# Performance work log

Hardware: AMD Instinct MI355X
Metric: run time of the kernel (lower is better)

Reference implementation:

```python
import jax, jax.numpy as jnp
import numpy as np

NOISE_LEVEL = 0.05
GAMMA = 0.2  # dt/tau


def setup_inputs() -> dict:
    key = jax.random.key(0)
    ks = jax.random.split(key, 4)
    B, T, I, L, O = 64, 512, 128, 1024, 128
    return {
        "input": jax.random.normal(ks[0], (B, T, I), dtype=jnp.float32),
        "noise": jax.random.normal(ks[1], (B, T, L), dtype=jnp.float32),
        "wi": jax.random.normal(ks[2], (I, L), dtype=jnp.float32),
        "si": jnp.ones((I,), dtype=jnp.float32),
        "wrec": jax.random.normal(ks[3], (L, L), dtype=jnp.float32) * (1.0 / np.sqrt(L)),
        "b": jnp.zeros((L,), dtype=jnp.float32),
        "wo": jax.random.normal(jax.random.fold_in(key, 7), (L, O), dtype=jnp.float32) * (1.0 / L),
        "so": jnp.ones((O,), dtype=jnp.float32),
        "h0": jnp.zeros((L,), dtype=jnp.float32),
    }


def reference(input, noise, wi, si, wrec, b, wo, so, h0):
    B = input.shape[0]
    # proxy parameters: wi_full = (wi.T * si).T == wi * si[:, None]; wo_full = wo * so
    wi_full = wi * si[:, None]          # (I, L)
    wo_full = wo * so                   # (L, O)

    h_init = jnp.broadcast_to(h0, (B, h0.shape[0]))  # (B, L)
    r_init = jnp.tanh(h_init)

    # Precompute input projections for all steps (no sequential dependency).
    u = jnp.einsum('bti,il->btl', input, wi_full)     # (B, T, L)

    def step(carry, xs):
        h, r = carry
        u_t, n_t = xs                                 # (B, L), (B, L)
        h = h + NOISE_LEVEL * n_t + GAMMA * (-h + r @ wrec.T + u_t)
        r = jnp.tanh(h + b)
        out_t = jnp.tanh(h) @ wo_full                 # (B, O)
        return (h, r), out_t

    xs = (jnp.swapaxes(u, 0, 1), jnp.swapaxes(noise, 0, 1))  # time-major
    _, out_t = jax.lax.scan(step, (h_init, r_init), xs)
    return jnp.swapaxes(out_t, 0, 1)                 # (B, T, O)
```

## Files before the change

### kernel.cpp

```cpp
#include <hip/hip_runtime.h>
#include <hip/hip_bf16.h>
#include <cstdint>
#include <cstddef>


static constexpr int B = 64, T = 512, I = 128, L = 1024, O = 128;
static constexpr float C_NOISE = 0.05f, C_GAMMA = 0.2f;

static constexpr int NROW = 4, BT = 16, NJB = 16, JT = 64;

static constexpr size_t WREC_OFF = 0;
static constexpr size_t WIT_OFF  = WREC_OFF + (size_t)L * L * 2;
static constexpr size_t WOT_OFF  = WIT_OFF + (size_t)L * I * 2;
static constexpr size_t RBUF_OFF = WOT_OFF + (size_t)O * L * 2;
static constexpr size_t FLAG_OFF = RBUF_OFF + (size_t)2 * B * L * 2;
static constexpr size_t NFLAGS   = (size_t)NROW * (T + 1) * NJB * 4;
static constexpr size_t FLAG_BYTES = NFLAGS * 4;
static constexpr size_t HBUF_OFF = ((FLAG_OFF + FLAG_BYTES + 511) / 512) * 512;
static constexpr size_t WS_NEED  = HBUF_OFF + (size_t)B * T * L * 2;

typedef __attribute__((ext_vector_type(8))) short s16x8;
typedef __attribute__((ext_vector_type(4))) float f32x4;
typedef __attribute__((ext_vector_type(4))) unsigned int u32x4;
typedef __attribute__((ext_vector_type(2))) unsigned long long u64x2;

__device__ __forceinline__ float fexp2(float x) {
#if __has_builtin(__builtin_amdgcn_exp2f)
  return __builtin_amdgcn_exp2f(x);
#else
  return exp2f(x);
#endif
}
__device__ __forceinline__ float frcp(float x) {
#if __has_builtin(__builtin_amdgcn_rcpf)
  return __builtin_amdgcn_rcpf(x);
#else
  return 1.0f / x;
#endif
}
__device__ __forceinline__ float fast_tanh(float x) {
  float e = fexp2(x * 2.8853900817779268f);
  return 1.0f - 2.0f * frcp(e + 1.0f);
}
__device__ __forceinline__ uint16_t bf16bits(float x) {
  __hip_bfloat16 h = __float2bfloat16(x);
  return *reinterpret_cast<uint16_t*>(&h);
}

__global__ void pack_kernel(const float* __restrict__ wi, const float* __restrict__ si,
                            const float* __restrict__ wrec,
                            const float* __restrict__ wo, const float* __restrict__ so,
                            uint8_t* __restrict__ ws) {
  int idx = blockIdx.x * blockDim.x + threadIdx.x;
  int stride = gridDim.x * blockDim.x;

  __hip_bfloat16* wrecb = (__hip_bfloat16*)(ws + WREC_OFF);
  for (int i = idx; i < L * L; i += stride) wrecb[i] = __float2bfloat16(wrec[i]);

  __hip_bfloat16* wit = (__hip_bfloat16*)(ws + WIT_OFF);
  for (int n = idx; n < L * I; n += stride) {
    int l = n >> 7, ii = n & 127;
    wit[n] = __float2bfloat16(wi[(size_t)ii * L + l] * si[ii]);
  }
  __hip_bfloat16* wot = (__hip_bfloat16*)(ws + WOT_OFF);
  for (int n = idx; n < O * L; n += stride) {
    int o = n >> 10, l = n & 1023;
    wot[n] = __float2bfloat16(wo[(size_t)l * O + o] * so[o]);
  }
  uint32_t* flags = (uint32_t*)(ws + FLAG_OFF);
  for (size_t n = idx; n < NFLAGS; n += stride) flags[n] = 0;
}

__launch_bounds__(256, 1)
__global__ void rnn_kernel(const float* __restrict__ input, const float* __restrict__ noise,
                           const float* __restrict__ bvec, const float* __restrict__ h0,
                           uint8_t* __restrict__ ws) {
  const int tid  = threadIdx.x;
  const int lane = tid & 63;
  const int w    = tid >> 6;
  const int bx   = blockIdx.x;
  const int row  = bx & 3;
  const int jblk = bx >> 2;
  const int b0   = row * BT;
  const int j0   = jblk * JT;
  const int l15  = lane & 15;
  const int lhi  = lane >> 4;

  const int jc0  = j0 + w * 16 + lhi * 4;
  const int mybatch = b0 + l15;

  const short* wrecb = (const short*)(ws + WREC_OFF);
  const short* wit   = (const short*)(ws + WIT_OFF);
  uint64_t* rbuf     = (uint64_t*)(ws + RBUF_OFF);
  uint32_t* flags    = (uint32_t*)(ws + FLAG_OFF);
  __hip_bfloat16* hbuf = (__hip_bfloat16*)(ws + HBUF_OFF);

  __shared__ __align__(16) uint8_t ldsA[2][16 * 2048];

  s16x8 wfrag[32];
  #pragma unroll
  for (int kt = 0; kt < 32; ++kt)
    wfrag[kt] = *(const s16x8*)(wrecb + (size_t)(j0 + w * 16 + l15) * L + kt * 32 + lhi * 8);
  s16x8 wifrag[4];
  #pragma unroll
  for (int kt = 0; kt < 4; ++kt)
    wifrag[kt] = *(const s16x8*)(wit + (size_t)(j0 + w * 16 + l15) * I + kt * 32 + lhi * 8);

  f32x4 bias, h;
  #pragma unroll
  for (int q = 0; q < 4; ++q) { bias[q] = bvec[jc0 + q]; h[q] = h0[jc0 + q]; }

  const int grow = tid >> 4;
  const int gseg = tid & 15;
  const int gsw  = (grow ^ gseg) & 7;

  {
    uint64_t pv = 0;
    #pragma unroll
    for (int q = 0; q < 4; ++q)
      pv |= (uint64_t)bf16bits(fast_tanh(h0[jc0 + q])) << (16 * q);
    size_t slot = (size_t)mybatch * (L / 4) + (size_t)(jc0 >> 2);
    __hip_atomic_store(&rbuf[slot], pv, __ATOMIC_RELAXED, __HIP_MEMORY_SCOPE_AGENT);
    __builtin_amdgcn_s_waitcnt(0);
    if (lane == 0)
      __hip_atomic_store(&flags[((size_t)(row * (T + 1) + 0) * NJB + jblk) * 4 + w], 1u,
                         __ATOMIC_RELAXED, __HIP_MEMORY_SCOPE_AGENT);
  }

  for (int t = 0; t < T; ++t) {
    f32x4 inLo[4], inHi[4];
    #pragma unroll
    for (int kt = 0; kt < 4; ++kt) {
      const float* p = input + ((size_t)(b0 + l15) * T + t) * I + kt * 32 + lhi * 8;
      inLo[kt] = *(const f32x4*)p;
      inHi[kt] = *(const f32x4*)(p + 4);
    }
    f32x4 nz = *(const f32x4*)(noise + ((size_t)mybatch * T + t) * L + jc0);
    s16x8 af[4];
    #pragma unroll
    for (int kt = 0; kt < 4; ++kt)
      #pragma unroll
      for (int q = 0; q < 4; ++q) {
        af[kt][q]     = (short)bf16bits(inLo[kt][q]);
        af[kt][q + 4] = (short)bf16bits(inHi[kt][q]);
      }

    f32x4 acc0 = {0.f,0.f,0.f,0.f}, acc1 = {0.f,0.f,0.f,0.f};
    f32x4 acc2 = {0.f,0.f,0.f,0.f}, acc3 = {0.f,0.f,0.f,0.f};
    acc0 = __builtin_amdgcn_mfma_f32_16x16x32_bf16(wifrag[0], af[0], acc0, 0, 0, 0);
    acc1 = __builtin_amdgcn_mfma_f32_16x16x32_bf16(wifrag[1], af[1], acc1, 0, 0, 0);
    acc2 = __builtin_amdgcn_mfma_f32_16x16x32_bf16(wifrag[2], af[2], acc2, 0, 0, 0);
    acc3 = __builtin_amdgcn_mfma_f32_16x16x32_bf16(wifrag[3], af[3], acc3, 0, 0, 0);

    {
      const uint32_t* fp = flags + ((size_t)(row * (T + 1) + t) * NJB + gseg) * 4;
      u32x4 f4;
      do {
        asm volatile("global_load_dwordx4 %0, %1, off sc0 sc1\n\ts_waitcnt vmcnt(0)"
                     : "=&v"(f4) : "v"(fp) : "memory");
      } while ((f4.x & f4.y & f4.z & f4.w) == 0u);
    }

    {
      const uint8_t* src = (const uint8_t*)rbuf
                         + (size_t)(t & 1) * (B * L * 2)
                         + (size_t)(b0 + grow) * 2048 + (size_t)gseg * 128;
      u64x2 v[8];
      #pragma unroll
      for (int i = 0; i < 8; ++i)
        asm volatile("global_load_dwordx4 %0, %1, off sc0 sc1"
                     : "=&v"(v[i]) : "v"(src + i * 16) : "memory");
      asm volatile("s_waitcnt vmcnt(0)" ::: "memory");
      __builtin_amdgcn_sched_barrier(0);
      uint8_t* dst = ldsA[t & 1] + grow * 2048 + gseg * 128;
      #pragma unroll
      for (int i = 0; i < 8; ++i)
        *(u64x2*)(dst + ((i ^ gsw) * 16)) = v[i];
    }
    __syncthreads();

    const uint8_t* Ab = ldsA[t & 1];
    #pragma unroll
    for (int kt = 0; kt < 32; ++kt) {
      int slot = ((kt * 4 + lhi) ^ ((l15 ^ (kt >> 1)) & 7)) * 16;
      s16x8 a = *(const s16x8*)(Ab + l15 * 2048 + slot);
      switch (kt & 3) {
        case 0: acc0 = __builtin_amdgcn_mfma_f32_16x16x32_bf16(wfrag[kt], a, acc0, 0, 0, 0); break;
        case 1: acc1 = __builtin_amdgcn_mfma_f32_16x16x32_bf16(wfrag[kt], a, acc1, 0, 0, 0); break;
        case 2: acc2 = __builtin_amdgcn_mfma_f32_16x16x32_bf16(wfrag[kt], a, acc2, 0, 0, 0); break;
        default: acc3 = __builtin_amdgcn_mfma_f32_16x16x32_bf16(wfrag[kt], a, acc3, 0, 0, 0); break;
      }
    }

    uint64_t pv = 0;
    #pragma unroll
    for (int q = 0; q < 4; ++q) {
      float hn = 0.8f * h[q] + C_GAMMA * ((acc0[q] + acc1[q]) + (acc2[q] + acc3[q]))
               + C_NOISE * nz[q];
      h[q] = hn;
      pv |= (uint64_t)bf16bits(fast_tanh(hn + bias[q])) << (16 * q);
    }
    {
      size_t slot = (size_t)((t + 1) & 1) * (B * L / 4)
                  + (size_t)mybatch * (L / 4) + (size_t)(jc0 >> 2);
      __hip_atomic_store(&rbuf[slot], pv, __ATOMIC_RELAXED, __HIP_MEMORY_SCOPE_AGENT);
    }
    __builtin_amdgcn_s_waitcnt(0);
    if (lane == 0)
      __hip_atomic_store(&flags[((size_t)(row * (T + 1) + (t + 1)) * NJB + jblk) * 4 + w], 1u,
                         __ATOMIC_RELAXED, __HIP_MEMORY_SCOPE_AGENT);

    {
      uint64_t hv = 0;
      #pragma unroll
      for (int q = 0; q < 4; ++q)
        hv |= (uint64_t)bf16bits(fast_tanh(h[q])) << (16 * q);
      *(uint64_t*)(hbuf + ((size_t)mybatch * T + t) * L + jc0) = hv;
    }
  }
}

__launch_bounds__(256)
__global__ void out_gemm(const uint8_t* __restrict__ ws, float* __restrict__ out) {
  const short* hs  = (const short*)(ws + HBUF_OFF);
  const short* wot = (const short*)(ws + WOT_OFF);
  const int tid = threadIdx.x, lane = tid & 63, w = tid >> 6;
  const int wm = w >> 1, wn = w & 1;
  const int l15 = lane & 15, lhi = lane >> 4;
  const size_t m0 = (size_t)blockIdx.x * 128 + (size_t)wm * 64;

  f32x4 acc[4][4] = {};
  for (int kt = 0; kt < 32; ++kt) {
    s16x8 a[4], b[4];
    #pragma unroll
    for (int fi = 0; fi < 4; ++fi)
      a[fi] = *(const s16x8*)(hs + (m0 + fi * 16 + l15) * L + kt * 32 + lhi * 8);
    #pragma unroll
    for (int fj = 0; fj < 4; ++fj)
      b[fj] = *(const s16x8*)(wot + (size_t)(wn * 64 + fj * 16 + l15) * L + kt * 32 + lhi * 8);
    #pragma unroll
    for (int fi = 0; fi < 4; ++fi)
      #pragma unroll
      for (int fj = 0; fj < 4; ++fj)
        acc[fi][fj] = __builtin_amdgcn_mfma_f32_16x16x32_bf16(a[fi], b[fj], acc[fi][fj], 0, 0, 0);
  }
  #pragma unroll
  for (int fi = 0; fi < 4; ++fi)
    #pragma unroll
    for (int fj = 0; fj < 4; ++fj)
      #pragma unroll
      for (int q = 0; q < 4; ++q) {
        size_t m = m0 + fi * 16 + lhi * 4 + q;
        out[m * O + wn * 64 + fj * 16 + l15] = acc[fi][fj][q];
      }
}

__global__ void ws_too_small(float* out, int n) {
  int i = blockIdx.x * blockDim.x + threadIdx.x;
  if (i < n) out[i] = 12345.0f;
}

extern "C" void kernel_launch(void* const* d_in, const int* in_sizes, int n_in,
                              void* d_out, int out_size, void* d_ws, size_t ws_size,
                              hipStream_t stream) {
  const float* input = (const float*)d_in[0];
  const float* noise = (const float*)d_in[1];
  const float* wi    = (const float*)d_in[2];
  const float* si    = (const float*)d_in[3];
  const float* wrec  = (const float*)d_in[4];
  const float* bvec  = (const float*)d_in[5];
  const float* wo    = (const float*)d_in[6];
  const float* so    = (const float*)d_in[7];
  const float* h0    = (const float*)d_in[8];
  uint8_t* ws = (uint8_t*)d_ws;
  float* out = (float*)d_out;

  if (ws_size < WS_NEED) {
    ws_too_small<<<(out_size + 255) / 256, 256, 0, stream>>>(out, out_size);
    return;
  }

  pack_kernel<<<256, 256, 0, stream>>>(wi, si, wrec, wo, so, ws);
  rnn_kernel<<<NROW * NJB, 256, 0, stream>>>(input, noise, bvec, h0, ws);
  out_gemm<<<(B * T) / 128, 256, 0, stream>>>(ws, out);
}
```

Baseline: 2.060 ms.

## Embed sequence-parity bit in recurrent state words, drop separate flag array

Replaces the per-step flag array and its spin-wait with data-embedded validity. The low bit of each packed bf16 state word now carries a phase bit, and consumers re-poll the state buffer until every word shows the expected phase. This removes the waitcnt-then-flag-store on the producer side and one round trip of flag polling on the consumer side. In exchange it perturbs the least significant mantissa bit of one bf16 value per word, and the spin loop has an iteration cap that could let stale data through.

```diff
diff --git a/kernel.cpp b/kernel.cpp
--- a/kernel.cpp
+++ b/kernel.cpp
@@ -13,15 +13,12 @@
 static constexpr size_t WIT_OFF  = WREC_OFF + (size_t)L * L * 2;
 static constexpr size_t WOT_OFF  = WIT_OFF + (size_t)L * I * 2;
 static constexpr size_t RBUF_OFF = WOT_OFF + (size_t)O * L * 2;
-static constexpr size_t FLAG_OFF = RBUF_OFF + (size_t)2 * B * L * 2;
-static constexpr size_t NFLAGS   = (size_t)NROW * (T + 1) * NJB * 4;
-static constexpr size_t FLAG_BYTES = NFLAGS * 4;
-static constexpr size_t HBUF_OFF = ((FLAG_OFF + FLAG_BYTES + 511) / 512) * 512;
+static constexpr size_t RBUF_BYTES = (size_t)2 * B * L * 2;
+static constexpr size_t HBUF_OFF = ((RBUF_OFF + RBUF_BYTES + 131072 + 511) / 512) * 512;
 static constexpr size_t WS_NEED  = HBUF_OFF + (size_t)B * T * L * 2;
 
 typedef __attribute__((ext_vector_type(8))) short s16x8;
 typedef __attribute__((ext_vector_type(4))) float f32x4;
-typedef __attribute__((ext_vector_type(4))) unsigned int u32x4;
 typedef __attribute__((ext_vector_type(2))) unsigned long long u64x2;
 
 __device__ __forceinline__ float fexp2(float x) {
@@ -67,8 +64,8 @@
     int o = n >> 10, l = n & 1023;
     wot[n] = __float2bfloat16(wo[(size_t)l * O + o] * so[o]);
   }
-  uint32_t* flags = (uint32_t*)(ws + FLAG_OFF);
-  for (size_t n = idx; n < NFLAGS; n += stride) flags[n] = 0;
+  uint32_t* rb = (uint32_t*)(ws + RBUF_OFF);
+  for (size_t n = idx; n < RBUF_BYTES / 4; n += stride) rb[n] = 0;
 }
 
 __launch_bounds__(256, 1)
@@ -92,7 +89,6 @@
   const short* wrecb = (const short*)(ws + WREC_OFF);
   const short* wit   = (const short*)(ws + WIT_OFF);
   uint64_t* rbuf     = (uint64_t*)(ws + RBUF_OFF);
-  uint32_t* flags    = (uint32_t*)(ws + FLAG_OFF);
   __hip_bfloat16* hbuf = (__hip_bfloat16*)(ws + HBUF_OFF);
 
   __shared__ __align__(16) uint8_t ldsA[2][16 * 2048];
@@ -119,12 +115,9 @@
     #pragma unroll
     for (int q = 0; q < 4; ++q)
       pv |= (uint64_t)bf16bits(fast_tanh(h0[jc0 + q])) << (16 * q);
+    pv = (pv & ~1ull) | 1ull;
     size_t slot = (size_t)mybatch * (L / 4) + (size_t)(jc0 >> 2);
     __hip_atomic_store(&rbuf[slot], pv, __ATOMIC_RELAXED, __HIP_MEMORY_SCOPE_AGENT);
-    __builtin_amdgcn_s_waitcnt(0);
-    if (lane == 0)
-      __hip_atomic_store(&flags[((size_t)(row * (T + 1) + 0) * NJB + jblk) * 4 + w], 1u,
-                         __ATOMIC_RELAXED, __HIP_MEMORY_SCOPE_AGENT);
   }
 
   for (int t = 0; t < T; ++t) {
@@ -152,25 +145,26 @@
     acc2 = __builtin_amdgcn_mfma_f32_16x16x32_bf16(wifrag[2], af[2], acc2, 0, 0, 0);
     acc3 = __builtin_amdgcn_mfma_f32_16x16x32_bf16(wifrag[3], af[3], acc3, 0, 0, 0);
 
+    u64x2 v[8];
     {
-      const uint32_t* fp = flags + ((size_t)(row * (T + 1) + t) * NJB + gseg) * 4;
-      u32x4 f4;
-      do {
-        asm volatile("global_load_dwordx4 %0, %1, off sc0 sc1\n\ts_waitcnt vmcnt(0)"
-                     : "=&v"(f4) : "v"(fp) : "memory");
-      } while ((f4.x & f4.y & f4.z & f4.w) == 0u);
-    }
-
-    {
+      const uint64_t want = (uint64_t)(((t >> 1) & 1) ^ 1);
       const uint8_t* src = (const uint8_t*)rbuf
                          + (size_t)(t & 1) * (B * L * 2)
                          + (size_t)(b0 + grow) * 2048 + (size_t)gseg * 128;
-      u64x2 v[8];
-      #pragma unroll
-      for (int i = 0; i < 8; ++i)
-        asm volatile("global_load_dwordx4 %0, %1, off sc0 sc1"
-                     : "=&v"(v[i]) : "v"(src + i * 16) : "memory");
-      asm volatile("s_waitcnt vmcnt(0)" ::: "memory");
+      uint32_t spin = 0;
+      uint64_t bad;
+      do {
+        #pragma unroll
+        for (int i = 0; i < 8; ++i)
+          asm volatile("global_load_dwordx4 %0, %1, off sc0 sc1"
+                       : "=&v"(v[i]) : "v"(src + i * 16) : "memory");
+        asm volatile("s_waitcnt vmcnt(0)" ::: "memory");
+        bad = 0;
+        #pragma unroll
+        for (int i = 0; i < 8; ++i)
+          bad |= (v[i].x ^ want) | (v[i].y ^ want);
+        bad &= 1ull;
+      } while (bad && (++spin < (1u << 18)));
       __builtin_amdgcn_sched_barrier(0);
       uint8_t* dst = ldsA[t & 1] + grow * 2048 + gseg * 128;
       #pragma unroll
@@ -201,14 +195,12 @@
       pv |= (uint64_t)bf16bits(fast_tanh(hn + bias[q])) << (16 * q);
     }
     {
+      const uint64_t sb = (uint64_t)((((t + 1) >> 1) & 1) ^ 1);
+      pv = (pv & ~1ull) | sb;
       size_t slot = (size_t)((t + 1) & 1) * (B * L / 4)
                   + (size_t)mybatch * (L / 4) + (size_t)(jc0 >> 2);
       __hip_atomic_store(&rbuf[slot], pv, __ATOMIC_RELAXED, __HIP_MEMORY_SCOPE_AGENT);
     }
-    __builtin_amdgcn_s_waitcnt(0);
-    if (lane == 0)
-      __hip_atomic_store(&flags[((size_t)(row * (T + 1) + (t + 1)) * NJB + jblk) * 4 + w], 1u,
-                         __ATOMIC_RELAXED, __HIP_MEMORY_SCOPE_AGENT);
 
     {
       uint64_t hv = 0;
```

Measured after the change: 2.052 ms. No clear change (-0.4%).
